# Kernel tuning notes

Hardware: AMD Instinct MI355X
Metric: run time of the kernel (lower is better)

## Reference

```python
import jax, jax.numpy as jnp
import numpy as np

B, P, S, CTX = 64, 10, 200, 512
H, NH, DH = 512, 4, 128      # hidden_dim, num_heads, head_dim
ROLE, NUMR = 32, 10
OUT = 2
T = 100                      # max_steps
LSTM_IN = OUT + 2 + ROLE + CTX  # 548


def setup_inputs() -> dict:
    key = jax.random.key(0)
    ks = jax.random.split(key, 32)
    std = 0.02
    f = jnp.float32
    inp = {
        'context_sequence': jax.random.normal(ks[0], (B, P, S, CTX), f),
        'initial_position': jax.random.normal(ks[1], (B, P, OUT), f),
        'ball_landing': jax.random.normal(ks[2], (B, OUT), f),
        'roles': jax.random.randint(ks[3], (B, P), 0, NUMR),
        'max_steps': T,
        # params
        'role_emb': jax.random.normal(ks[4], (NUMR, ROLE), f) * std,
        'Wc': jax.random.normal(ks[5], (H, CTX), f) * std,
        'bc': jnp.zeros((H,), f),
        'Wq': jax.random.normal(ks[6], (H, H), f) * std,
        'bq': jnp.zeros((H,), f),
        'Wk': jax.random.normal(ks[7], (H, H), f) * std,
        'bk': jnp.zeros((H,), f),
        'Wv': jax.random.normal(ks[8], (H, H), f) * std,
        'bv': jnp.zeros((H,), f),
        'Wo': jax.random.normal(ks[9], (H, H), f) * std,
        'bo': jnp.zeros((H,), f),
        'W_ih0': jax.random.normal(ks[10], (4 * H, LSTM_IN), f) * std,
        'W_hh0': jax.random.normal(ks[11], (4 * H, H), f) * std,
        'b_ih0': jnp.zeros((4 * H,), f),
        'b_hh0': jnp.zeros((4 * H,), f),
        'W_ih1': jax.random.normal(ks[12], (4 * H, H), f) * std,
        'W_hh1': jax.random.normal(ks[13], (4 * H, H), f) * std,
        'b_ih1': jnp.zeros((4 * H,), f),
        'b_hh1': jnp.zeros((4 * H,), f),
        'Wf1': jax.random.normal(ks[14], (H // 2, H), f) * std,
        'bf1': jnp.zeros((H // 2,), f),
        'Wf2': jax.random.normal(ks[15], (OUT, H // 2), f) * std,
        'bf2': jnp.zeros((OUT,), f),
    }
    return inp


def _lstm_cell(x, h, c, Wih, Whh, bih, bhh):
    # torch gate order: i, f, g, o
    g = x @ Wih.T + bih + h @ Whh.T + bhh
    i, fg, gg, o = jnp.split(g, 4, axis=-1)
    cn = jax.nn.sigmoid(fg) * c + jax.nn.sigmoid(i) * jnp.tanh(gg)
    hn = jax.nn.sigmoid(o) * jnp.tanh(cn)
    return hn, cn


def reference(context_sequence, initial_position, ball_landing, roles, max_steps,
              role_emb, Wc, bc, Wq, bq, Wk, bk, Wv, bv, Wo, bo,
              W_ih0, W_hh0, b_ih0, b_hh0, W_ih1, W_hh1, b_ih1, b_hh1,
              Wf1, bf1, Wf2, bf2):
    b, p, s, ctx = context_sequence.shape
    n = b * p
    dt = context_sequence.dtype
    scale = 1.0 / np.sqrt(DH)

    # project context once; hoist K,V (keys/values are constant across steps)
    ctx_proj = context_sequence.reshape(n, s, ctx) @ Wc.T + bc          # [N,S,H]
    K = (ctx_proj @ Wk.T + bk).reshape(n, s, NH, DH)                    # [N,S,h,d]
    V = (ctx_proj @ Wv.T + bv).reshape(n, s, NH, DH)

    role_e = role_emb[roles.reshape(-1)]                                # [N,ROLE]
    ball = jnp.broadcast_to(ball_landing[:, None, :], (b, p, OUT)).reshape(n, OUT)
    pos0 = initial_position.reshape(n, OUT)
    h0 = jnp.zeros((2, n, H), dt)
    c0 = jnp.zeros((2, n, H), dt)

    def step(carry, _):
        h, c, pos = carry
        # query: current pos zero-padded to context_dim, then context_proj
        qin = jnp.concatenate([pos, jnp.zeros((n, ctx - OUT), dt)], axis=-1)
        qp = qin @ Wc.T + bc                                            # [N,H]
        q = (qp @ Wq.T + bq).reshape(n, NH, DH)
        scores = jnp.einsum('nhd,nshd->nhs', q, K) * scale
        w = jax.nn.softmax(scores, axis=-1)
        att = jnp.einsum('nhs,nshd->nhd', w, V).reshape(n, H)
        att = att @ Wo.T + bo                                           # [N,H]
        x = jnp.concatenate([pos, ball, role_e, att], axis=-1)          # [N,548]
        h0n, c0n = _lstm_cell(x, h[0], c[0], W_ih0, W_hh0, b_ih0, b_hh0)
        h1n, c1n = _lstm_cell(h0n, h[1], c[1], W_ih1, W_hh1, b_ih1, b_hh1)
        hid = jax.nn.relu(h1n @ Wf1.T + bf1)
        nxt = hid @ Wf2.T + bf2                                         # [N,2]
        return (jnp.stack([h0n, h1n]), jnp.stack([c0n, c1n]), nxt), nxt

    _, preds = jax.lax.scan(step, (h0, c0, pos0), None, length=max_steps)
    # [T,N,2] -> [B,P,T,2]
    return preds.transpose(1, 0, 2).reshape(b, p, max_steps, OUT)
```

## Files before the change

### kernel.cpp

```cpp
#include <hip/hip_runtime.h>
#include <hip/hip_bf16.h>
#include <cstddef>


typedef _Float16 hx8 __attribute__((ext_vector_type(8)));
typedef float fx4 __attribute__((ext_vector_type(4)));

#define NSEQ 640
#define TSTEPS 100
#define XC0 1088
#define XC1 1024
#define NBLK 640
#define FL 32

__device__ __forceinline__ float sigm(float x){ return 1.0f/(1.0f+__expf(-x)); }
__device__ __forceinline__ float tanh_(float x){
  x = fminf(fmaxf(x, -15.0f), 15.0f);
  float e = __expf(2.0f*x);
  return (e-1.0f)/(e+1.0f);
}
__device__ __forceinline__ float sel4(float a0,float a1,float a2,float a3,int h){
  float r = a0; r = (h==1)?a1:r; r = (h==2)?a2:r; r = (h==3)?a3:r; return r;
}


__global__ void kF1(const float* __restrict__ Wq, const float* __restrict__ Wc,
                    const float* __restrict__ bc, const float* __restrict__ bq,
                    float* __restrict__ u){
  int r = blockIdx.x*256 + threadIdx.x; if (r >= 512) return;
  float s0=0.f, s1=0.f, s2=0.f;
  for (int k=0;k<512;k++){
    float wq = Wq[r*512+k];
    s0 += wq*Wc[k*512+0];
    s1 += wq*Wc[k*512+1];
    s2 += wq*bc[k];
  }
  u[r]=s0; u[512+r]=s1; u[1024+r]=s2+bq[r];
}

__global__ __launch_bounds__(512) void kF2a(const float* __restrict__ Wk,
                                            const float* __restrict__ u,
                                            float* __restrict__ z){
  int ih = blockIdx.x; int kk = threadIdx.x;
  int i = ih>>2, h = ih&3;
  float s = 0.f;
  for (int d=0; d<128; d++)
    s += Wk[(h*128+d)*512 + kk] * u[i*512 + h*128 + d];
  z[ih*512+kk] = s;
}

__global__ __launch_bounds__(512) void kF2b(const float* __restrict__ z,
                                            const float* __restrict__ Wc,
                                            const float* __restrict__ bc,
                                            const float* __restrict__ bk,
                                            const float* __restrict__ u,
                                            float* __restrict__ Y, float* __restrict__ cc){
  const float scale = 0.08838834764831845f;
  int ih = blockIdx.x; int j = threadIdx.x;
  int i = ih>>2, h = ih&3;
  float s = 0.f;
  for (int kk=0;kk<512;kk++) s += z[ih*512+kk]*Wc[kk*512+j];
  Y[ih*512+j] = s*scale;
  if (j==0){
    float t=0.f;
    for (int kk=0;kk<512;kk++) t += z[ih*512+kk]*bc[kk];
    for (int d=0;d<128;d++) t += u[i*512+h*128+d]*bk[h*128+d];
    cc[ih] = t*scale;
  }
}

__global__ void kFbv(const float* __restrict__ Wv, const float* __restrict__ bc,
                     const float* __restrict__ bv, float* __restrict__ bv2){
  int r = blockIdx.x*256 + threadIdx.x; if (r >= 512) return;
  float s = bv[r];
  for (int k=0;k<512;k++) s += Wv[r*512+k]*bc[k];
  bv2[r]=s;
}

__global__ __launch_bounds__(256) void kgemm(const float* __restrict__ A, int lda, int aoff,
                                             const float* __restrict__ B, int ldb,
                                             float* __restrict__ C, int ldc, int K){
  __shared__ float As[64][16];
  __shared__ float Bs[16][64];
  int tid = threadIdx.x; int tx = tid&15, ty = tid>>4;
  int bx = blockIdx.x, by = blockIdx.y;
  float acc[4][4];
#pragma unroll
  for (int i=0;i<4;i++)
#pragma unroll
    for (int j=0;j<4;j++) acc[i][j]=0.f;
  for (int kk=0; kk<K; kk+=16){
#pragma unroll
    for (int e=0;e<4;e++){
      int id = tid*4+e;
      int r = id>>4, c = id&15;
      As[r][c] = A[(size_t)(by*64+r)*lda + aoff + kk + c];
      int r2 = id>>6, c2 = id&63;
      Bs[r2][c2] = B[(size_t)(kk+r2)*ldb + bx*64 + c2];
    }
    __syncthreads();
#pragma unroll
    for (int k=0;k<16;k++){
      float bvv[4];
#pragma unroll
      for (int j=0;j<4;j++) bvv[j] = Bs[k][tx*4+j];
#pragma unroll
      for (int i=0;i<4;i++){
        float av = As[ty*4+i][k];
#pragma unroll
        for (int j=0;j<4;j++) acc[i][j] += av*bvv[j];
      }
    }
    __syncthreads();
  }
#pragma unroll
  for (int i=0;i<4;i++)
#pragma unroll
    for (int j=0;j<4;j++)
      C[(size_t)(by*64+ty*4+i)*ldc + bx*64+tx*4+j] = acc[i][j];
}

__global__ void ktransp(const float* __restrict__ A, float* __restrict__ AT){
  int idx = blockIdx.x*256 + threadIdx.x;
  int r = idx>>9, c = idx&511;
  AT[c*512 + r] = A[idx];
}

__global__ void kbcat0(const float* __restrict__ Wih0, const float* __restrict__ Wmix,
                       const float* __restrict__ Whh0, _Float16* __restrict__ B){
  int r = blockIdx.x;
  for (int c = threadIdx.x; c < 1088; c += 256){
    float v;
    if (c < 36) v = Wih0[r*548 + c];
    else if (c < 548) v = Wmix[r*512 + (c-36)];
    else if (c < 576) v = 0.f;
    else v = Whh0[r*512 + (c-576)];
    B[(size_t)r*1088 + c] = (_Float16)v;
  }
}

__global__ void kbcat1(const float* __restrict__ Wih1, const float* __restrict__ Whh1,
                       _Float16* __restrict__ B){
  int r = blockIdx.x;
  for (int c = threadIdx.x; c < 1024; c += 256){
    float v = (c < 512) ? Wih1[r*512 + c] : Whh1[r*512 + (c-512)];
    B[(size_t)r*1024 + c] = (_Float16)v;
  }
}

__global__ void kcast(const float* __restrict__ s, _Float16* __restrict__ d, int n){
  int i = blockIdx.x*256 + threadIdx.x;
  if (i < n) d[i] = (_Float16)s[i];
}

__global__ void kbias(const float* __restrict__ Wih0, const float* __restrict__ bo,
                      const float* __restrict__ bih0, const float* __restrict__ bhh0,
                      const float* __restrict__ bih1, const float* __restrict__ bhh1,
                      float* __restrict__ b0, float* __restrict__ b1){
  int j = blockIdx.x*256 + threadIdx.x; if (j >= 2048) return;
  float s = bih0[j]+bhh0[j];
  for (int k=0;k<512;k++) s += Wih0[j*548+36+k]*bo[k];
  b0[j]=s; b1[j]=bih1[j]+bhh1[j];
}


__global__ __launch_bounds__(256) void kP1(const float* __restrict__ ctx,
                                           const float* __restrict__ Y,
                                           const float* __restrict__ cc,
                                           float* __restrict__ W6){
  __shared__ float Yl[6144];
  __shared__ float ccl[12];
  int tid = threadIdx.x; int n = blockIdx.x;
  for (int e = tid; e < 6144; e += 256) Yl[e] = Y[e];
  if (tid < 12) ccl[tid] = cc[tid];
  __syncthreads();
  int wave = tid >> 6, lane = tid & 63;
  for (int it = 0; it < 50; ++it){
    int s = it*4 + wave;
    const float* cp = ctx + ((size_t)n*200 + s)*512;
    float p[12];
#pragma unroll
    for (int i=0;i<12;i++) p[i]=0.f;
    for (int c8 = 0; c8 < 8; ++c8){
      int col = c8*64 + lane;
      float v = cp[col];
#pragma unroll
      for (int i=0;i<12;i++) p[i] += v * Yl[i*512+col];
    }
#pragma unroll
    for (int m = 32; m; m >>= 1){
#pragma unroll
      for (int i=0;i<12;i++) p[i] += __shfl_xor(p[i], m, 64);
    }
    if (lane < 4){
      int h = lane;
      float a  = sel4(p[0],p[1],p[2], p[3], h) + ccl[h];
      float b  = sel4(p[4],p[5],p[6], p[7], h) + ccl[4+h];
      float cp_= sel4(p[8],p[9],p[10],p[11],h) + ccl[8+h];
      float beta = __expf(cp_);
      size_t base = (size_t)(n*24 + h*6)*200 + s;
      W6[base + 0*200] = beta;
      W6[base + 1*200] = beta*a;
      W6[base + 2*200] = beta*b;
      W6[base + 3*200] = beta*a*a*0.5f;
      W6[base + 4*200] = beta*a*b;
      W6[base + 5*200] = beta*b*b*0.5f;
    }
  }
}

__global__ __launch_bounds__(256) void kP2(const float* __restrict__ ctx,
                                           const float* __restrict__ W6,
                                           float* __restrict__ F, float* __restrict__ S){
  __shared__ float w6[4800];
  int tid = threadIdx.x, n = blockIdx.x;
  for (int e = tid; e < 4800; e += 256) w6[e] = W6[(size_t)n*4800 + e];
  __syncthreads();
  float a0[24], a1[24];
#pragma unroll
  for (int r=0;r<24;r++){ a0[r]=0.f; a1[r]=0.f; }
  const float* cp = ctx + (size_t)n*200*512;
  for (int s=0;s<200;s++){
    float v0 = cp[s*512 + tid];
    float v1 = cp[s*512 + tid + 256];
#pragma unroll
    for (int r=0;r<24;r++){ float w = w6[r*200+s]; a0[r]+=w*v0; a1[r]+=w*v1; }
  }
#pragma unroll
  for (int r=0;r<24;r++){
    F[(size_t)(n*24+r)*512 + tid]       = a0[r];
    F[(size_t)(n*24+r)*512 + tid + 256] = a1[r];
  }
  if (tid < 24){
    float s=0.f;
    for (int ss=0; ss<200; ss++) s += w6[tid*200+ss];
    S[n*24+tid]=s;
  }
}

__global__ __launch_bounds__(128) void kP3(const float* __restrict__ F,
                                           const float* __restrict__ WcvT,
                                           float* __restrict__ M){
  __shared__ float Fl[3072];
  int tid = threadIdx.x; int b = blockIdx.x; int n = b>>2, h = b&3;
  for (int e = tid; e < 3072; e += 128) Fl[e] = F[(size_t)(n*24 + h*6)*512 + e];
  __syncthreads();
  float acc[6];
#pragma unroll
  for (int i=0;i<6;i++) acc[i]=0.f;
  for (int k=0;k<512;k++){
    float w = WcvT[k*512 + h*128 + tid];
#pragma unroll
    for (int i=0;i<6;i++) acc[i] += w * Fl[i*512+k];
  }
#pragma unroll
  for (int i=0;i<6;i++) M[(size_t)(n*24+h*6+i)*128 + tid] = acc[i];
}


__global__ __launch_bounds__(512) void kinit(const float* __restrict__ ball,
                    const int* __restrict__ roles, const float* __restrict__ remb,
                    _Float16* __restrict__ x0, _Float16* __restrict__ x1,
                    _Float16* __restrict__ hc0, _Float16* __restrict__ hc1,
                    float* __restrict__ c0, float* __restrict__ c1,
                    unsigned* __restrict__ bar){
  int n = blockIdx.x, tid = threadIdx.x;
  int b = n/10;
  int role = roles[n];
  for (int c = tid; c < XC0; c += 512){
    float v = 0.f;
    if (c>=2 && c<4)       v = ball[b*2 + (c-2)];
    else if (c>=4 && c<36) v = remb[role*32 + (c-4)];
    _Float16 hv = (_Float16)v;
    x0[(size_t)n*XC0+c] = hv;
    x1[(size_t)n*XC0+c] = hv;
  }
  for (int c = tid; c < XC1; c += 512){
    hc0[(size_t)n*XC1+c] = (_Float16)0.f;
    hc1[(size_t)n*XC1+c] = (_Float16)0.f;
  }
  for (int e = tid; e < 512; e += 512){
    c0[n*512+e]=0.f; c1[n*512+e]=0.f;
  }
  if (tid < FL) bar[n*FL + tid] = 0u;
  if (n == 0 && tid >= 128 && tid < 128+FL)
    bar[NBLK*FL + (tid-128)] = 0u;
}

__global__ __launch_bounds__(128) void katt0(const float* __restrict__ ipos,
                                             const float* __restrict__ M,
                                             const float* __restrict__ S,
                                             const float* __restrict__ bv2,
                                             _Float16* __restrict__ x){
  int n = blockIdx.x, tid = threadIdx.x;
  float p0 = ipos[n*2], p1 = ipos[n*2+1];
  if (tid==0){ x[(size_t)n*XC0]=(_Float16)p0; x[(size_t)n*XC0+1]=(_Float16)p1; }
  float fa=p0*p0, fb=p0*p1, fc=p1*p1;
  for (int hd = tid; hd < 512; hd += 128){
    int h = hd>>7;
    int sb = n*24 + h*6;
    float den = S[sb] + p0*S[sb+1] + p1*S[sb+2] + fa*S[sb+3] + fb*S[sb+4] + fc*S[sb+5];
    const float* mp = M + (size_t)sb*128 + (hd&127);
    float num = mp[0] + p0*mp[128] + p1*mp[256] + fa*mp[384] + fb*mp[512] + fc*mp[640];
    x[(size_t)n*XC0 + 36 + hd] = (_Float16)(num/den + bv2[hd]);
  }
}


__device__ __forceinline__ void gates_body(
    const _Float16* __restrict__ A, int lda, int nc,
    const _Float16* __restrict__ B,
    const float* __restrict__ bias, float* __restrict__ cst,
    _Float16* __restrict__ h1p, int ldh1, int co1,
    _Float16* __restrict__ h2p, int ldh2, int co2,
    int bx, _Float16* sbase, float (*eps)[32][16]){
  int tid = threadIdx.x, w = tid>>6, lane = tid&63;
  int lr = lane&15, lq = lane>>4;
  int mblk = bx>>5, jb = bx&31;
  int m0 = mblk*32, j0 = jb*16;
  int li = lane>>3, lc = lane&7;
  const _Float16* gA  = A + (size_t)(m0 + w*8 + li)*lda + lc*8;
  const _Float16* gB0 = B + (size_t)(w*512 + j0 + li)*lda + lc*8;
  const _Float16* gB1 = B + (size_t)(w*512 + j0 + 8 + li)*lda + lc*8;
  int sA  = (w*8 + li)*64        + ((lc ^ li)<<3);
  int sB0 = 2048 + (w*16 + li)*64 + ((lc ^ li)<<3);
  int sB1 = 2048 + (w*16 + 8 + li)*64 + ((lc ^ li)<<3);
  int ra7 = lr & 7;
  int fA00 = lr*64        + (((lq  ) ^ ra7)<<3);
  int fA01 = lr*64        + (((lq+4) ^ ra7)<<3);
  int fA10 = (16+lr)*64   + (((lq  ) ^ ra7)<<3);
  int fA11 = (16+lr)*64   + (((lq+4) ^ ra7)<<3);
  int fB0  = 2048 + (w*16+lr)*64 + (((lq  ) ^ ra7)<<3);
  int fB1  = 2048 + (w*16+lr)*64 + (((lq+4) ^ ra7)<<3);
  hx8 rA  = *(const hx8*)(gA);
  hx8 rB0 = *(const hx8*)(gB0);
  hx8 rB1 = *(const hx8*)(gB1);
  fx4 ac0={0.f,0.f,0.f,0.f}, ac1={0.f,0.f,0.f,0.f};
  for (int c=0; c<nc; ++c){
    _Float16* sb = sbase + (c&1)*6144;
    *(hx8*)(sb + sA)  = rA;
    *(hx8*)(sb + sB0) = rB0;
    *(hx8*)(sb + sB1) = rB1;
    __syncthreads();
    if (c+1 < nc){
      int k = (c+1)*64;
      rA  = *(const hx8*)(gA  + k);
      rB0 = *(const hx8*)(gB0 + k);
      rB1 = *(const hx8*)(gB1 + k);
    }
    hx8 b0 = *(const hx8*)(sb + fB0);
    hx8 a0 = *(const hx8*)(sb + fA00);
    hx8 a1 = *(const hx8*)(sb + fA10);
    ac0 = __builtin_amdgcn_mfma_f32_16x16x32_f16(a0, b0, ac0, 0,0,0);
    ac1 = __builtin_amdgcn_mfma_f32_16x16x32_f16(a1, b0, ac1, 0,0,0);
    hx8 b1  = *(const hx8*)(sb + fB1);
    hx8 a0b = *(const hx8*)(sb + fA01);
    hx8 a1b = *(const hx8*)(sb + fA11);
    ac0 = __builtin_amdgcn_mfma_f32_16x16x32_f16(a0b, b1, ac0, 0,0,0);
    ac1 = __builtin_amdgcn_mfma_f32_16x16x32_f16(a1b, b1, ac1, 0,0,0);
  }
#pragma unroll
  for (int r=0;r<4;r++){
    eps[w][lq*4+r][lr]    = ac0[r];
    eps[w][16+lq*4+r][lr] = ac1[r];
  }
  __syncthreads();
#pragma unroll
  for (int e=0;e<2;e++){
    int idx = e*256 + tid;
    int ml = idx>>4, j = idx&15;
    float gi = eps[0][ml][j] + bias[       j0+j];
    float gf = eps[1][ml][j] + bias[ 512 + j0+j];
    float gg = eps[2][ml][j] + bias[1024 + j0+j];
    float go = eps[3][ml][j] + bias[1536 + j0+j];
    int ci = (m0+ml)*512 + j0 + j;
    float c_ = cst[ci];
    float cn = sigm(gf)*c_ + sigm(gi)*tanh_(gg);
    float hn = sigm(go)*tanh_(cn);
    cst[ci] = cn;
    _Float16 hh = (_Float16)hn;
    h1p[(size_t)(m0+ml)*ldh1 + co1 + j0 + j] = hh;
    if (h2p) h2p[(size_t)(m0+ml)*ldh2 + co2 + j0 + j] = hh;
  }
}

__global__ __launch_bounds__(256) void kgates(
    const _Float16* __restrict__ A, int lda, int nc,
    const _Float16* __restrict__ B,
    const float* __restrict__ bias, float* __restrict__ cst,
    _Float16* __restrict__ h1p, int ldh1, int co1,
    _Float16* __restrict__ h2p, int ldh2, int co2){
  __shared__ __align__(16) char smem[32768];
  gates_body(A, lda, nc, B, bias, cst, h1p, ldh1, co1, h2p, ldh2, co2,
             blockIdx.x, (_Float16*)smem, (float(*)[32][16])(smem + 24576));
}

__device__ __forceinline__ void s3_body(const _Float16* __restrict__ h1, int ldh,
    const _Float16* __restrict__ Wf1, const float* __restrict__ bf1,
    const float* __restrict__ Wf2, const float* __restrict__ bf2,
    const float* __restrict__ M, const float* __restrict__ S,
    const float* __restrict__ bv2, _Float16* __restrict__ xn,
    float* __restrict__ out, int t, int n0,
    float (*hid)[264], float (*posL)[2], float (*denL)[4]){
  int tid = threadIdx.x, w = tid>>6, lane = tid&63;
  int lr = lane&15, lq = lane>>4;
  fx4 acc[4];
#pragma unroll
  for (int c=0;c<4;c++) acc[c] = (fx4){0.f,0.f,0.f,0.f};
  {
    const _Float16* ap = h1 + (size_t)(n0+lr)*ldh + lq*8;
    for (int ks=0; ks<16; ks++){
      hx8 a = *(const hx8*)(ap + ks*32);
#pragma unroll
      for (int c=0;c<4;c++){
        const _Float16* bp = Wf1 + (size_t)(w*64 + c*16 + lr)*512 + ks*32 + lq*8;
        acc[c] = __builtin_amdgcn_mfma_f32_16x16x32_f16(a, *(const hx8*)bp, acc[c], 0,0,0);
      }
    }
  }
#pragma unroll
  for (int c=0;c<4;c++)
#pragma unroll
    for (int r=0;r<4;r++){
      int col = w*64 + c*16 + lr;
      hid[lq*4+r][col] = fmaxf(acc[c][r] + bf1[col], 0.f);
    }
  __syncthreads();
  {
    int nn = tid>>4, o = (tid>>3)&1, sub = tid&7;
    float s = 0.f;
#pragma unroll
    for (int k2=0;k2<32;k2++) s += hid[nn][k2*8 + sub] * Wf2[o*256 + k2*8 + sub];
    s += __shfl_xor(s, 1, 64);
    s += __shfl_xor(s, 2, 64);
    s += __shfl_xor(s, 4, 64);
    if (sub==0){
      s += bf2[o];
      out[((size_t)(n0+nn)*TSTEPS + t)*2 + o] = s;
      posL[nn][o] = s;
      xn[(size_t)(n0+nn)*XC0 + o] = (_Float16)s;
    }
  }
  __syncthreads();
  if (tid < 64){
    int nn = tid>>2, h = tid&3;
    float p0 = posL[nn][0], p1 = posL[nn][1];
    int sb = (n0+nn)*24 + h*6;
    float den = S[sb] + p0*S[sb+1] + p1*S[sb+2] + p0*p0*S[sb+3] + p0*p1*S[sb+4] + p1*p1*S[sb+5];
    denL[nn][h] = 1.0f/den;
  }
  __syncthreads();
#pragma unroll
  for (int half=0; half<2; half++){
    int hd = half*256 + tid;
    int h = hd>>7, d = hd&127;
    for (int nn=0; nn<16; nn++){
      float p0 = posL[nn][0], p1 = posL[nn][1];
      float fa = p0*p0, fb = p0*p1, fc = p1*p1;
      const float* mp = M + (size_t)((n0+nn)*24 + h*6)*128 + d;
      float num = mp[0] + p0*mp[128] + p1*mp[256] + fa*mp[384] + fb*mp[512] + fc*mp[640];
      xn[(size_t)(n0+nn)*XC0 + 36 + hd] = (_Float16)(num*denL[nn][h] + bv2[hd]);
    }
  }
}

__global__ __launch_bounds__(256) void ks3b(const _Float16* __restrict__ h1, int ldh,
    const _Float16* __restrict__ Wf1, const float* __restrict__ bf1,
    const float* __restrict__ Wf2, const float* __restrict__ bf2,
    const float* __restrict__ M, const float* __restrict__ S,
    const float* __restrict__ bv2, _Float16* __restrict__ xn,
    float* __restrict__ out, int t){
  __shared__ float hid[16][264];
  __shared__ float posL[16][2];
  __shared__ float denL[16][4];
  s3_body(h1, ldh, Wf1, bf1, Wf2, bf2, M, S, bv2, xn, out, t,
          blockIdx.x*16, hid, posL, denL);
}


__device__ __forceinline__ void gbar(unsigned* bar, int bid, unsigned val){
  __syncthreads();
  unsigned* gen = bar + NBLK*FL;
  if (bid == 0){
    for (int i = 1 + (int)threadIdx.x; i < NBLK; i += 256){
      while (__hip_atomic_load(bar + (size_t)i*FL, __ATOMIC_RELAXED,
                               __HIP_MEMORY_SCOPE_AGENT) < val)
        __builtin_amdgcn_s_sleep(4);
    }
    __threadfence();
    __syncthreads();
    if (threadIdx.x == 0)
      __hip_atomic_store(gen, val, __ATOMIC_RELEASE, __HIP_MEMORY_SCOPE_AGENT);
  } else {
    if (threadIdx.x == 0){
      __hip_atomic_store(bar + (size_t)bid*FL, val, __ATOMIC_RELEASE,
                         __HIP_MEMORY_SCOPE_AGENT);
      while (__hip_atomic_load(gen, __ATOMIC_RELAXED,
                               __HIP_MEMORY_SCOPE_AGENT) < val)
        __builtin_amdgcn_s_sleep(4);
      (void)__hip_atomic_load(gen, __ATOMIC_ACQUIRE, __HIP_MEMORY_SCOPE_AGENT);
    }
  }
  __syncthreads();
}

struct LoopArgs {
  const _Float16* B0; const _Float16* B1;
  const float* b0; const float* b1;
  float* c0; float* c1;
  _Float16* x0; _Float16* x1; _Float16* h0; _Float16* h1;
  const _Float16* Wf1; const float* bf1; const float* Wf2; const float* bf2;
  const float* M; const float* S; const float* bv2;
  float* out; unsigned* bar;
};

__global__ __launch_bounds__(256, 3) void kloop(LoopArgs a){
  __shared__ __align__(16) char smem[32768];
  _Float16* sbase = (_Float16*)smem;
  float (*eps)[32][16] = (float(*)[32][16])(smem + 24576);
  float (*hid)[264] = (float(*)[264])smem;
  float (*posL)[2] = (float(*)[2])(smem + 16896);
  float (*denL)[4] = (float(*)[4])(smem + 17024);
  int bid = blockIdx.x;
  for (int t = 0; t < TSTEPS; ++t){
    unsigned bb = (unsigned)(t*3);
    _Float16* xin = (t&1) ? a.x1 : a.x0;
    _Float16* xnx = (t&1) ? a.x0 : a.x1;
    _Float16* hin = (t&1) ? a.h1 : a.h0;
    _Float16* hnx = (t&1) ? a.h0 : a.h1;
    gates_body(xin, XC0, 17, a.B0, a.b0, a.c0, hin, XC1, 0, xnx, XC0, 576,
               bid, sbase, eps);
    gbar(a.bar, bid, bb+1);
    gates_body(hin, XC1, 16, a.B1, a.b1, a.c1, hnx, XC1, 512,
               (_Float16*)0, 0, 0, bid, sbase, eps);
    gbar(a.bar, bid, bb+2);
    if (bid < 40)
      s3_body(hnx + 512, XC1, a.Wf1, a.bf1, a.Wf2, a.bf2, a.M, a.S, a.bv2,
              xnx, a.out, t, bid*16, hid, posL, denL);
    gbar(a.bar, bid, bb+3);
  }
}


extern "C" void kernel_launch(void* const* d_in, const int* in_sizes, int n_in,
                              void* d_out, int out_size, void* d_ws, size_t ws_size,
                              hipStream_t stream) {
  const float* ctx   = (const float*)d_in[0];
  const float* ipos  = (const float*)d_in[1];
  const float* ball  = (const float*)d_in[2];
  const int*   roles = (const int*)  d_in[3];
  const float* remb  = (const float*)d_in[5];
  const float* Wc    = (const float*)d_in[6];
  const float* bc    = (const float*)d_in[7];
  const float* Wq    = (const float*)d_in[8];
  const float* bq    = (const float*)d_in[9];
  const float* Wk    = (const float*)d_in[10];
  const float* bk    = (const float*)d_in[11];
  const float* Wv    = (const float*)d_in[12];
  const float* bv    = (const float*)d_in[13];
  const float* Wo    = (const float*)d_in[14];
  const float* bo    = (const float*)d_in[15];
  const float* Wih0  = (const float*)d_in[16];
  const float* Whh0  = (const float*)d_in[17];
  const float* bih0  = (const float*)d_in[18];
  const float* bhh0  = (const float*)d_in[19];
  const float* Wih1  = (const float*)d_in[20];
  const float* Whh1  = (const float*)d_in[21];
  const float* bih1  = (const float*)d_in[22];
  const float* bhh1  = (const float*)d_in[23];
  const float* Wf1   = (const float*)d_in[24];
  const float* bf1   = (const float*)d_in[25];
  const float* Wf2   = (const float*)d_in[26];
  const float* bf2   = (const float*)d_in[27];
  float* out = (float*)d_out;

  char* w = (char*)d_ws;
  auto alloc = [&](size_t bytes){ void* p = (void*)w; w += (bytes + 255) & ~(size_t)255; return p; };
  float* fY    = (float*)alloc(12*512*4);
  float* fcc   = (float*)alloc(12*4);
  float* fu    = (float*)alloc(3*512*4);
  float* fz    = (float*)alloc(12*512*4);
  float* fbv2  = (float*)alloc(512*4);
  float* fWcv  = (float*)alloc((size_t)512*512*4);
  float* fWcvT = (float*)alloc((size_t)512*512*4);
  float* fWmix = (float*)alloc((size_t)2048*512*4);
  _Float16* hB0  = (_Float16*)alloc((size_t)2048*XC0*2);
  _Float16* hB1  = (_Float16*)alloc((size_t)2048*XC1*2);
  _Float16* hWf1 = (_Float16*)alloc((size_t)256*512*2);
  float* fb0 = (float*)alloc(2048*4);
  float* fb1 = (float*)alloc(2048*4);
  float* fW6 = (float*)alloc((size_t)NSEQ*24*200*4);
  float* fS  = (float*)alloc((size_t)NSEQ*24*4);
  float* fF  = (float*)alloc((size_t)NSEQ*24*512*4);
  float* fM  = (float*)alloc((size_t)NSEQ*24*128*4);
  _Float16* xc0 = (_Float16*)alloc((size_t)NSEQ*XC0*2);
  _Float16* xc1 = (_Float16*)alloc((size_t)NSEQ*XC0*2);
  _Float16* hc0 = (_Float16*)alloc((size_t)NSEQ*XC1*2);
  _Float16* hc1 = (_Float16*)alloc((size_t)NSEQ*XC1*2);
  float* fc0 = (float*)alloc((size_t)NSEQ*512*4);
  float* fc1 = (float*)alloc((size_t)NSEQ*512*4);
  unsigned* bar = (unsigned*)alloc((size_t)(NBLK+1)*FL*4);

  kF1 <<<2,  256, 0, stream>>>(Wq, Wc, bc, bq, fu);
  kF2a<<<12, 512, 0, stream>>>(Wk, fu, fz);
  kF2b<<<12, 512, 0, stream>>>(fz, Wc, bc, bk, fu, fY, fcc);
  kFbv<<<2,  256, 0, stream>>>(Wv, bc, bv, fbv2);
  kgemm<<<dim3(8,8),  256, 0, stream>>>(Wv,   512, 0,  Wc, 512, fWcv,  512, 512);
  ktransp<<<1024, 256, 0, stream>>>(fWcv, fWcvT);
  kgemm<<<dim3(8,32), 256, 0, stream>>>(Wih0, 548, 36, Wo, 512, fWmix, 512, 512);
  kbcat0<<<2048, 256, 0, stream>>>(Wih0, fWmix, Whh0, hB0);
  kbcat1<<<2048, 256, 0, stream>>>(Wih1, Whh1, hB1);
  kcast<<<512,  256, 0, stream>>>(Wf1, hWf1, 256*512);
  kbias<<<8, 256, 0, stream>>>(Wih0, bo, bih0, bhh0, bih1, bhh1, fb0, fb1);

  kP1<<<NSEQ, 256, 0, stream>>>(ctx, fY, fcc, fW6);
  kP2<<<NSEQ, 256, 0, stream>>>(ctx, fW6, fF, fS);
  kP3<<<NSEQ*4, 128, 0, stream>>>(fF, fWcvT, fM);

  kinit<<<NSEQ, 512, 0, stream>>>(ball, roles, remb, xc0, xc1, hc0, hc1, fc0, fc1, bar);
  katt0<<<NSEQ, 128, 0, stream>>>(ipos, fM, fS, fbv2, xc0);

  int maxb = 0;
  hipError_t qe = hipOccupancyMaxActiveBlocksPerMultiprocessor(
      &maxb, reinterpret_cast<const void*>(kloop), 256, 0);
  if (qe == hipSuccess && maxb >= 3){
    LoopArgs la;
    la.B0 = hB0; la.B1 = hB1; la.b0 = fb0; la.b1 = fb1;
    la.c0 = fc0; la.c1 = fc1;
    la.x0 = xc0; la.x1 = xc1; la.h0 = hc0; la.h1 = hc1;
    la.Wf1 = hWf1; la.bf1 = bf1; la.Wf2 = Wf2; la.bf2 = bf2;
    la.M = fM; la.S = fS; la.bv2 = fbv2; la.out = out; la.bar = bar;
    kloop<<<NBLK, 256, 0, stream>>>(la);
  } else {
    for (int t = 0; t < TSTEPS; ++t){
      _Float16* xin  = (t&1) ? xc1 : xc0;
      _Float16* xnx  = (t&1) ? xc0 : xc1;
      _Float16* hin  = (t&1) ? hc1 : hc0;
      _Float16* hnx  = (t&1) ? hc0 : hc1;
      kgates<<<640, 256, 0, stream>>>(xin, XC0, 17, hB0, fb0, fc0,
                                      hin, XC1, 0, xnx, XC0, 576);
      kgates<<<640, 256, 0, stream>>>(hin, XC1, 16, hB1, fb1, fc1,
                                      hnx, XC1, 512, (_Float16*)nullptr, 0, 0);
      ks3b<<<40, 256, 0, stream>>>(hnx + 512, XC1, hWf1, bf1, Wf2, bf2,
                                   fM, fS, fbv2, xnx, out, t);
    }
  }
}
```

Measured before the change: 4.810 ms.

## Replace grid-wide barrier with per-row-block flag barriers and deepen gate prefetch

Replaces the centralized grid barrier (block 0 polls all flags, then broadcasts a generation word) with local barriers where each block waits only on the 32 blocks sharing its 32-row batch slice, polled in parallel by one wavefront with a ballot. Only the two blocks per slice that run the output-head stage wait after the layer-1 gates, and the head's rows are remapped to that slice. The gate GEMM loop becomes templated on chunk count, fully unrolled, with a 3-deep register prefetch. Activations produced by other blocks are now read via relaxed agent-scope atomic loads so cached stale data is not used. This relies on the data dependencies really being confined to row slices, and the atomic loads may be slower than plain vector loads.

After: 5.110 ms. 1.06x slower.

```diff
diff --git a/kernel.cpp b/kernel.cpp
--- a/kernel.cpp
+++ b/kernel.cpp
@@ -5,6 +5,7 @@
 
 typedef _Float16 hx8 __attribute__((ext_vector_type(8)));
 typedef float fx4 __attribute__((ext_vector_type(4)));
+typedef unsigned long long u64;
 
 #define NSEQ 640
 #define TSTEPS 100
@@ -21,6 +22,13 @@
 }
 __device__ __forceinline__ float sel4(float a0,float a1,float a2,float a3,int h){
   float r = a0; r = (h==1)?a1:r; r = (h==2)?a2:r; r = (h==3)?a3:r; return r;
+}
+
+__device__ __forceinline__ hx8 ldA(const _Float16* p){
+  u64 q0 = __hip_atomic_load((u64*)p,     __ATOMIC_RELAXED, __HIP_MEMORY_SCOPE_AGENT);
+  u64 q1 = __hip_atomic_load((u64*)p + 1, __ATOMIC_RELAXED, __HIP_MEMORY_SCOPE_AGENT);
+  union { u64 q[2]; hx8 v; } u; u.q[0]=q0; u.q[1]=q1;
+  return u.v;
 }
 
 
@@ -283,8 +291,6 @@
     c0[n*512+e]=0.f; c1[n*512+e]=0.f;
   }
   if (tid < FL) bar[n*FL + tid] = 0u;
-  if (n == 0 && tid >= 128 && tid < 128+FL)
-    bar[NBLK*FL + (tid-128)] = 0u;
 }
 
 __global__ __launch_bounds__(128) void katt0(const float* __restrict__ ipos,
@@ -307,8 +313,9 @@
 }
 
 
+template<int NC>
 __device__ __forceinline__ void gates_body(
-    const _Float16* __restrict__ A, int lda, int nc,
+    const _Float16* __restrict__ A, int lda,
     const _Float16* __restrict__ B,
     const float* __restrict__ bias, float* __restrict__ cst,
     _Float16* __restrict__ h1p, int ldh1, int co1,
@@ -332,21 +339,28 @@
   int fA11 = (16+lr)*64   + (((lq+4) ^ ra7)<<3);
   int fB0  = 2048 + (w*16+lr)*64 + (((lq  ) ^ ra7)<<3);
   int fB1  = 2048 + (w*16+lr)*64 + (((lq+4) ^ ra7)<<3);
-  hx8 rA  = *(const hx8*)(gA);
-  hx8 rB0 = *(const hx8*)(gB0);
-  hx8 rB1 = *(const hx8*)(gB1);
+  hx8 pA[3], pB0[3], pB1[3];
+#pragma unroll
+  for (int i=0;i<3;i++){
+    int k = i*64;
+    pA[i]  = ldA(gA + k);
+    pB0[i] = *(const hx8*)(gB0 + k);
+    pB1[i] = *(const hx8*)(gB1 + k);
+  }
   fx4 ac0={0.f,0.f,0.f,0.f}, ac1={0.f,0.f,0.f,0.f};
-  for (int c=0; c<nc; ++c){
+#pragma unroll
+  for (int c=0; c<NC; ++c){
+    const int s = c % 3;
     _Float16* sb = sbase + (c&1)*6144;
-    *(hx8*)(sb + sA)  = rA;
-    *(hx8*)(sb + sB0) = rB0;
-    *(hx8*)(sb + sB1) = rB1;
+    *(hx8*)(sb + sA)  = pA[s];
+    *(hx8*)(sb + sB0) = pB0[s];
+    *(hx8*)(sb + sB1) = pB1[s];
     __syncthreads();
-    if (c+1 < nc){
-      int k = (c+1)*64;
-      rA  = *(const hx8*)(gA  + k);
-      rB0 = *(const hx8*)(gB0 + k);
-      rB1 = *(const hx8*)(gB1 + k);
+    if (c+3 < NC){
+      int k = (c+3)*64;
+      pA[s]  = ldA(gA + k);
+      pB0[s] = *(const hx8*)(gB0 + k);
+      pB1[s] = *(const hx8*)(gB1 + k);
     }
     hx8 b0 = *(const hx8*)(sb + fB0);
     hx8 a0 = *(const hx8*)(sb + fA00);
@@ -384,15 +398,15 @@
   }
 }
 
+template<int NC>
 __global__ __launch_bounds__(256) void kgates(
-    const _Float16* __restrict__ A, int lda, int nc,
-    const _Float16* __restrict__ B,
-    const float* __restrict__ bias, float* __restrict__ cst,
-    _Float16* __restrict__ h1p, int ldh1, int co1,
-    _Float16* __restrict__ h2p, int ldh2, int co2){
+    const _Float16* A, int lda, const _Float16* B,
+    const float* bias, float* cst,
+    _Float16* h1p, int ldh1, int co1,
+    _Float16* h2p, int ldh2, int co2){
   __shared__ __align__(16) char smem[32768];
-  gates_body(A, lda, nc, B, bias, cst, h1p, ldh1, co1, h2p, ldh2, co2,
-             blockIdx.x, (_Float16*)smem, (float(*)[32][16])(smem + 24576));
+  gates_body<NC>(A, lda, B, bias, cst, h1p, ldh1, co1, h2p, ldh2, co2,
+                 blockIdx.x, (_Float16*)smem, (float(*)[32][16])(smem + 24576));
 }
 
 __device__ __forceinline__ void s3_body(const _Float16* __restrict__ h1, int ldh,
@@ -410,7 +424,7 @@
   {
     const _Float16* ap = h1 + (size_t)(n0+lr)*ldh + lq*8;
     for (int ks=0; ks<16; ks++){
-      hx8 a = *(const hx8*)(ap + ks*32);
+      hx8 a = ldA(ap + ks*32);
 #pragma unroll
       for (int c=0;c<4;c++){
         const _Float16* bp = Wf1 + (size_t)(w*64 + c*16 + lr)*512 + ks*32 + lq*8;
@@ -478,30 +492,27 @@
 }
 
 
-__device__ __forceinline__ void gbar(unsigned* bar, int bid, unsigned val){
-  __syncthreads();
-  unsigned* gen = bar + NBLK*FL;
-  if (bid == 0){
-    for (int i = 1 + (int)threadIdx.x; i < NBLK; i += 256){
-      while (__hip_atomic_load(bar + (size_t)i*FL, __ATOMIC_RELAXED,
-                               __HIP_MEMORY_SCOPE_AGENT) < val)
-        __builtin_amdgcn_s_sleep(4);
-    }
-    __threadfence();
-    __syncthreads();
-    if (threadIdx.x == 0)
-      __hip_atomic_store(gen, val, __ATOMIC_RELEASE, __HIP_MEMORY_SCOPE_AGENT);
-  } else {
-    if (threadIdx.x == 0){
-      __hip_atomic_store(bar + (size_t)bid*FL, val, __ATOMIC_RELEASE,
-                         __HIP_MEMORY_SCOPE_AGENT);
-      while (__hip_atomic_load(gen, __ATOMIC_RELAXED,
-                               __HIP_MEMORY_SCOPE_AGENT) < val)
-        __builtin_amdgcn_s_sleep(4);
-      (void)__hip_atomic_load(gen, __ATOMIC_ACQUIRE, __HIP_MEMORY_SCOPE_AGENT);
-    }
-  }
-  __syncthreads();
+__device__ __forceinline__ void garrive(unsigned* bar, int bx, unsigned val){
+  __syncthreads();
+  if (threadIdx.x == 0)
+    __hip_atomic_store(bar + (size_t)bx*FL, val, __ATOMIC_RELEASE,
+                       __HIP_MEMORY_SCOPE_AGENT);
+}
+__device__ __forceinline__ void gwait(unsigned* bar, int bx, unsigned val){
+  if (threadIdx.x < 64){
+    const unsigned* fp = bar + (size_t)((bx & ~31) + (threadIdx.x & 31))*FL;
+    for(;;){
+      unsigned v = __hip_atomic_load((unsigned*)fp, __ATOMIC_RELAXED,
+                                     __HIP_MEMORY_SCOPE_AGENT);
+      if (__ballot(v >= val) == ~0ull) break;
+      __builtin_amdgcn_s_sleep(2);
+    }
+  }
+  __syncthreads();
+}
+__device__ __forceinline__ void gbar32(unsigned* bar, int bx, unsigned val){
+  garrive(bar, bx, val);
+  gwait(bar, bx, val);
 }
 
 struct LoopArgs {
@@ -522,22 +533,24 @@
   float (*posL)[2] = (float(*)[2])(smem + 16896);
   float (*denL)[4] = (float(*)[4])(smem + 17024);
   int bid = blockIdx.x;
+  int mblk = bid>>5, jb = bid&31;
   for (int t = 0; t < TSTEPS; ++t){
     unsigned bb = (unsigned)(t*3);
     _Float16* xin = (t&1) ? a.x1 : a.x0;
     _Float16* xnx = (t&1) ? a.x0 : a.x1;
     _Float16* hin = (t&1) ? a.h1 : a.h0;
     _Float16* hnx = (t&1) ? a.h0 : a.h1;
-    gates_body(xin, XC0, 17, a.B0, a.b0, a.c0, hin, XC1, 0, xnx, XC0, 576,
-               bid, sbase, eps);
-    gbar(a.bar, bid, bb+1);
-    gates_body(hin, XC1, 16, a.B1, a.b1, a.c1, hnx, XC1, 512,
-               (_Float16*)0, 0, 0, bid, sbase, eps);
-    gbar(a.bar, bid, bb+2);
-    if (bid < 40)
+    gates_body<17>(xin, XC0, a.B0, a.b0, a.c0, hin, XC1, 0, xnx, XC0, 576,
+                   bid, sbase, eps);
+    gbar32(a.bar, bid, bb+1);
+    gates_body<16>(hin, XC1, a.B1, a.b1, a.c1, hnx, XC1, 512,
+                   (_Float16*)0, 0, 0, bid, sbase, eps);
+    if (jb < 2){
+      gbar32(a.bar, bid, bb+2);
       s3_body(hnx + 512, XC1, a.Wf1, a.bf1, a.Wf2, a.bf2, a.M, a.S, a.bv2,
-              xnx, a.out, t, bid*16, hid, posL, denL);
-    gbar(a.bar, bid, bb+3);
+              xnx, a.out, t, mblk*32 + jb*16, hid, posL, denL);
+    }
+    gbar32(a.bar, bid, bb+3);
   }
 }
 
@@ -637,10 +650,10 @@
       _Float16* xnx  = (t&1) ? xc0 : xc1;
       _Float16* hin  = (t&1) ? hc1 : hc0;
       _Float16* hnx  = (t&1) ? hc0 : hc1;
-      kgates<<<640, 256, 0, stream>>>(xin, XC0, 17, hB0, fb0, fc0,
-                                      hin, XC1, 0, xnx, XC0, 576);
-      kgates<<<640, 256, 0, stream>>>(hin, XC1, 16, hB1, fb1, fc1,
-                                      hnx, XC1, 512, (_Float16*)nullptr, 0, 0);
+      kgates<17><<<640, 256, 0, stream>>>(xin, XC0, hB0, fb0, fc0,
+                                          hin, XC1, 0, xnx, XC0, 576);
+      kgates<16><<<640, 256, 0, stream>>>(hin, XC1, hB1, fb1, fc1,
+                                          hnx, XC1, 512, (_Float16*)nullptr, 0, 0);
       ks3b<<<40, 256, 0, stream>>>(hnx + 512, XC1, hWf1, bf1, Wf2, bf2,
                                    fM, fS, fbv2, xnx, out, t);
     }
```
